# Kernel optimization log

Measured on AMD Instinct MI355X. Metric: run time of the kernel, lower is better.

The kernel has to match this reference:

```python
import jax, jax.numpy as jnp
import numpy as np

N = 2097152  # batch of 3x3 matrices


def setup_inputs() -> dict:
    key = jax.random.key(0)
    k1, k2 = jax.random.split(key)
    rotation = jax.random.normal(k1, (N, 3, 3), dtype=jnp.float32)
    # learned parameter: eye(3) + 1e-3 * randn, per __init__
    mat = jnp.eye(3, dtype=jnp.float32) + 0.001 * jax.random.normal(k2, (3, 3), dtype=jnp.float32)
    return {"rotation": rotation, "mat": mat}


def reference(rotation, mat):
    # new_mat = mat @ rotation (mat broadcast over batch)  -> [N,3,3]
    new_mat = jnp.einsum('ab,nbc->nac', mat, rotation)
    # polar rotation factor via batched 3x3 SVD: R = U @ V^T
    U, S, Vh = jnp.linalg.svd(new_mat, full_matrices=False)
    out = jnp.einsum('nab,nbc->nac', U, Vh)  # torch: U @ V.transpose == U @ Vh
    logdet = jnp.zeros((rotation.shape[0],), dtype=rotation.dtype)
    return out, logdet
```

## Files before the change

### kernel.cpp

```cpp
#include <hip/hip_runtime.h>
#include <math.h>


typedef float v2f __attribute__((ext_vector_type(2)));

#define NEWTON_ITERS 6
#define NS_ITERS 2

__global__ __launch_bounds__(256) void polar3x3_pk_kernel(
    const float* __restrict__ rot,
    const float* __restrict__ mat,
    float* __restrict__ out,
    int n)
{
    __shared__ float lds[4608];
    const int t = threadIdx.x;
    const long long base = (long long)blockIdx.x * 512;
    const bool full = (base + 512 <= (long long)n);

    if (full) {
        const float4* s4 = (const float4*)(rot + base * 9);
        float4* l4 = (float4*)lds;
        #pragma unroll
        for (int k = 0; k < 5; ++k) {
            int idx = t + 256 * k;
            if (idx < 1152) l4[idx] = s4[idx];
        }
    } else {
        for (int j = t; j < 4608; j += 256) {
            long long g = base * 9 + j;
            lds[j] = (g < (long long)n * 9) ? rot[g] : 0.0f;
        }
    }
    __syncthreads();

    const float* L = lds + t * 18;
    v2f r00 = {L[0], L[9]},  r01 = {L[1], L[10]}, r02 = {L[2], L[11]};
    v2f r10 = {L[3], L[12]}, r11 = {L[4], L[13]}, r12 = {L[5], L[14]};
    v2f r20 = {L[6], L[15]}, r21 = {L[7], L[16]}, r22 = {L[8], L[17]};

    const float m00 = mat[0], m01 = mat[1], m02 = mat[2];
    const float m10 = mat[3], m11 = mat[4], m12 = mat[5];
    const float m20 = mat[6], m21 = mat[7], m22 = mat[8];

    v2f x00 = m00*r00 + m01*r10 + m02*r20;
    v2f x01 = m00*r01 + m01*r11 + m02*r21;
    v2f x02 = m00*r02 + m01*r12 + m02*r22;
    v2f x10 = m10*r00 + m11*r10 + m12*r20;
    v2f x11 = m10*r01 + m11*r11 + m12*r21;
    v2f x12 = m10*r02 + m11*r12 + m12*r22;
    v2f x20 = m20*r00 + m21*r10 + m22*r20;
    v2f x21 = m20*r01 + m21*r11 + m22*r21;
    v2f x22 = m20*r02 + m21*r12 + m22*r22;

    #pragma unroll
    for (int it = 0; it < NEWTON_ITERS; ++it) {
        v2f c00 = x11*x22 - x12*x21;
        v2f c01 = x12*x20 - x10*x22;
        v2f c02 = x10*x21 - x11*x20;
        v2f c10 = x02*x21 - x01*x22;
        v2f c11 = x00*x22 - x02*x20;
        v2f c12 = x01*x20 - x00*x21;
        v2f c20 = x01*x12 - x02*x11;
        v2f c21 = x02*x10 - x00*x12;
        v2f c22 = x00*x11 - x01*x10;

        v2f det = x00*c00 + x01*c01 + x02*c02;

        float d0 = det.x, d1 = det.y;
        float ad0 = fmaxf(fabsf(d0), 1e-30f);
        float ad1 = fmaxf(fabsf(d1), 1e-30f);
        float z0 = __builtin_amdgcn_exp2f(__builtin_amdgcn_logf(ad0) * (-1.0f/3.0f));
        float z1 = __builtin_amdgcn_exp2f(__builtin_amdgcn_logf(ad1) * (-1.0f/3.0f));
        v2f s = {0.5f * z0, 0.5f * z1};
        v2f u = {copysignf(0.5f * z0 * z0, d0), copysignf(0.5f * z1 * z1, d1)};

        x00 = s*x00 + u*c00;  x01 = s*x01 + u*c01;  x02 = s*x02 + u*c02;
        x10 = s*x10 + u*c10;  x11 = s*x11 + u*c11;  x12 = s*x12 + u*c12;
        x20 = s*x20 + u*c20;  x21 = s*x21 + u*c21;  x22 = s*x22 + u*c22;
    }

    #pragma unroll
    for (int it = 0; it < NS_ITERS; ++it) {
        v2f s00 = x00*x00 + x10*x10 + x20*x20;
        v2f s01 = x00*x01 + x10*x11 + x20*x21;
        v2f s02 = x00*x02 + x10*x12 + x20*x22;
        v2f s11 = x01*x01 + x11*x11 + x21*x21;
        v2f s12 = x01*x02 + x11*x12 + x21*x22;
        v2f s22 = x02*x02 + x12*x12 + x22*x22;
        v2f t00 = 1.5f - 0.5f*s00, t01 = -0.5f*s01, t02 = -0.5f*s02;
        v2f t11 = 1.5f - 0.5f*s11, t12 = -0.5f*s12;
        v2f t22 = 1.5f - 0.5f*s22;
        v2f y00 = x00*t00 + x01*t01 + x02*t02;
        v2f y01 = x00*t01 + x01*t11 + x02*t12;
        v2f y02 = x00*t02 + x01*t12 + x02*t22;
        v2f y10 = x10*t00 + x11*t01 + x12*t02;
        v2f y11 = x10*t01 + x11*t11 + x12*t12;
        v2f y12 = x10*t02 + x11*t12 + x12*t22;
        v2f y20 = x20*t00 + x21*t01 + x22*t02;
        v2f y21 = x20*t01 + x21*t11 + x22*t12;
        v2f y22 = x20*t02 + x21*t12 + x22*t22;
        x00=y00; x01=y01; x02=y02;
        x10=y10; x11=y11; x12=y12;
        x20=y20; x21=y21; x22=y22;
    }

    float* S = lds + t * 18;
    S[0]=x00.x; S[9]=x00.y;  S[1]=x01.x; S[10]=x01.y;  S[2]=x02.x; S[11]=x02.y;
    S[3]=x10.x; S[12]=x10.y; S[4]=x11.x; S[13]=x11.y;  S[5]=x12.x; S[14]=x12.y;
    S[6]=x20.x; S[15]=x20.y; S[7]=x21.x; S[16]=x21.y;  S[8]=x22.x; S[17]=x22.y;
    __syncthreads();

    if (full) {
        float4* d4 = (float4*)(out + base * 9);
        const float4* l4 = (const float4*)lds;
        #pragma unroll
        for (int k = 0; k < 5; ++k) {
            int idx = t + 256 * k;
            if (idx < 1152) d4[idx] = l4[idx];
        }
        if (t < 128) {
            float4* ld4 = (float4*)(out + (long long)n * 9 + base);
            ld4[t] = make_float4(0.f, 0.f, 0.f, 0.f);
        }
    } else {
        for (int j = t; j < 4608; j += 256) {
            long long g = base * 9 + j;
            if (g < (long long)n * 9) out[g] = lds[j];
        }
        for (int j = t; j < 512; j += 256) {
            long long i2 = base + j;
            if (i2 < (long long)n) out[(long long)n * 9 + i2] = 0.0f;
        }
    }
}

extern "C" void kernel_launch(void* const* d_in, const int* in_sizes, int n_in,
                              void* d_out, int out_size, void* d_ws, size_t ws_size,
                              hipStream_t stream) {
    const float* rot = (const float*)d_in[0];
    const float* mat = (const float*)d_in[1];
    float* out = (float*)d_out;

    int n = in_sizes[0] / 9;
    int block = 256;
    int grid = (n + 511) / 512;
    polar3x3_pk_kernel<<<grid, block, 0, stream>>>(rot, mat, out, n);
}
```

Measured before the change: 32.33 us.

## Stage input per wavefront via global_load_lds and drop block barriers

Each wavefront now stages its own 128 matrices into a private LDS slice using direct global-to-LDS loads. This replaces the block-wide cooperative copy and removes both __syncthreads, relying on wave-local s_waitcnt instead. Output is written back through the wave's LDS slice with nontemporal vector stores. The tail path uses direct per-thread global access. This cuts block-level synchronisation and register staging, at the cost of relying on the semantics of global_load_lds and on intra-wave LDS ordering without an explicit barrier.

After: 29.70 us. 1.09x faster.

```diff
diff --git a/kernel.cpp b/kernel.cpp
--- a/kernel.cpp
+++ b/kernel.cpp
@@ -3,56 +3,16 @@
 
 
 typedef float v2f __attribute__((ext_vector_type(2)));
+typedef float v4f __attribute__((ext_vector_type(4)));
 
 #define NEWTON_ITERS 6
 #define NS_ITERS 2
 
-__global__ __launch_bounds__(256) void polar3x3_pk_kernel(
-    const float* __restrict__ rot,
-    const float* __restrict__ mat,
-    float* __restrict__ out,
-    int n)
+__device__ __forceinline__ void polar_pair(
+    v2f& x00, v2f& x01, v2f& x02,
+    v2f& x10, v2f& x11, v2f& x12,
+    v2f& x20, v2f& x21, v2f& x22)
 {
-    __shared__ float lds[4608];
-    const int t = threadIdx.x;
-    const long long base = (long long)blockIdx.x * 512;
-    const bool full = (base + 512 <= (long long)n);
-
-    if (full) {
-        const float4* s4 = (const float4*)(rot + base * 9);
-        float4* l4 = (float4*)lds;
-        #pragma unroll
-        for (int k = 0; k < 5; ++k) {
-            int idx = t + 256 * k;
-            if (idx < 1152) l4[idx] = s4[idx];
-        }
-    } else {
-        for (int j = t; j < 4608; j += 256) {
-            long long g = base * 9 + j;
-            lds[j] = (g < (long long)n * 9) ? rot[g] : 0.0f;
-        }
-    }
-    __syncthreads();
-
-    const float* L = lds + t * 18;
-    v2f r00 = {L[0], L[9]},  r01 = {L[1], L[10]}, r02 = {L[2], L[11]};
-    v2f r10 = {L[3], L[12]}, r11 = {L[4], L[13]}, r12 = {L[5], L[14]};
-    v2f r20 = {L[6], L[15]}, r21 = {L[7], L[16]}, r22 = {L[8], L[17]};
-
-    const float m00 = mat[0], m01 = mat[1], m02 = mat[2];
-    const float m10 = mat[3], m11 = mat[4], m12 = mat[5];
-    const float m20 = mat[6], m21 = mat[7], m22 = mat[8];
-
-    v2f x00 = m00*r00 + m01*r10 + m02*r20;
-    v2f x01 = m00*r01 + m01*r11 + m02*r21;
-    v2f x02 = m00*r02 + m01*r12 + m02*r22;
-    v2f x10 = m10*r00 + m11*r10 + m12*r20;
-    v2f x11 = m10*r01 + m11*r11 + m12*r21;
-    v2f x12 = m10*r02 + m11*r12 + m12*r22;
-    v2f x20 = m20*r00 + m21*r10 + m22*r20;
-    v2f x21 = m20*r01 + m21*r11 + m22*r21;
-    v2f x22 = m20*r02 + m21*r12 + m22*r22;
-
     #pragma unroll
     for (int it = 0; it < NEWTON_ITERS; ++it) {
         v2f c00 = x11*x22 - x12*x21;
@@ -104,33 +64,108 @@
         x10=y10; x11=y11; x12=y12;
         x20=y20; x21=y21; x22=y22;
     }
+}
 
-    float* S = lds + t * 18;
-    S[0]=x00.x; S[9]=x00.y;  S[1]=x01.x; S[10]=x01.y;  S[2]=x02.x; S[11]=x02.y;
-    S[3]=x10.x; S[12]=x10.y; S[4]=x11.x; S[13]=x11.y;  S[5]=x12.x; S[14]=x12.y;
-    S[6]=x20.x; S[15]=x20.y; S[7]=x21.x; S[16]=x21.y;  S[8]=x22.x; S[17]=x22.y;
-    __syncthreads();
+__global__ __launch_bounds__(256) void polar3x3_wave_kernel(
+    const float* __restrict__ rot,
+    const float* __restrict__ mat,
+    float* __restrict__ out,
+    int n)
+{
+    __shared__ float lds[4608];
+    const int t    = threadIdx.x;
+    const int lane = t & 63;
+    const int w    = t >> 6;
+    const long long blockBase = (long long)blockIdx.x * 512;
+    const long long waveBase  = blockBase + (long long)w * 128;
+    float* wlds = lds + w * 1152;
+
+    const float m00 = mat[0], m01 = mat[1], m02 = mat[2];
+    const float m10 = mat[3], m11 = mat[4], m12 = mat[5];
+    const float m20 = mat[6], m21 = mat[7], m22 = mat[8];
+
+    const bool full = (blockBase + 512 <= (long long)n);
+
+    v2f r00, r01, r02, r10, r11, r12, r20, r21, r22;
 
     if (full) {
-        float4* d4 = (float4*)(out + base * 9);
-        const float4* l4 = (const float4*)lds;
+        const float* gsrc = rot + waveBase * 9;
         #pragma unroll
-        for (int k = 0; k < 5; ++k) {
-            int idx = t + 256 * k;
-            if (idx < 1152) d4[idx] = l4[idx];
+        for (int k = 0; k < 4; ++k) {
+            __builtin_amdgcn_global_load_lds(
+                (const __attribute__((address_space(1))) void*)(gsrc + k * 256 + lane * 4),
+                (__attribute__((address_space(3))) void*)(wlds + k * 256),
+                16, 0, 0);
         }
-        if (t < 128) {
-            float4* ld4 = (float4*)(out + (long long)n * 9 + base);
-            ld4[t] = make_float4(0.f, 0.f, 0.f, 0.f);
+        #pragma unroll
+        for (int k = 0; k < 2; ++k) {
+            __builtin_amdgcn_global_load_lds(
+                (const __attribute__((address_space(1))) void*)(gsrc + 1024 + k * 64 + lane),
+                (__attribute__((address_space(3))) void*)(wlds + 1024 + k * 64),
+                4, 0, 0);
         }
+        asm volatile("s_waitcnt vmcnt(0)" ::: "memory");
+
+        const float* L = wlds + lane * 18;
+        r00 = v2f{L[0], L[9]};  r01 = v2f{L[1], L[10]}; r02 = v2f{L[2], L[11]};
+        r10 = v2f{L[3], L[12]}; r11 = v2f{L[4], L[13]}; r12 = v2f{L[5], L[14]};
+        r20 = v2f{L[6], L[15]}; r21 = v2f{L[7], L[16]}; r22 = v2f{L[8], L[17]};
     } else {
-        for (int j = t; j < 4608; j += 256) {
-            long long g = base * 9 + j;
-            if (g < (long long)n * 9) out[g] = lds[j];
+        #pragma unroll
+        for (int q = 0; q < 2; ++q) {
+            long long mi = waveBase + 2 * lane + q;
+            if (mi < (long long)n) {
+                const float* r = rot + mi * 9;
+                r00[q]=r[0]; r01[q]=r[1]; r02[q]=r[2];
+                r10[q]=r[3]; r11[q]=r[4]; r12[q]=r[5];
+                r20[q]=r[6]; r21[q]=r[7]; r22[q]=r[8];
+            } else {
+                r00[q]=1.f; r01[q]=0.f; r02[q]=0.f;
+                r10[q]=0.f; r11[q]=1.f; r12[q]=0.f;
+                r20[q]=0.f; r21[q]=0.f; r22[q]=1.f;
+            }
         }
-        for (int j = t; j < 512; j += 256) {
-            long long i2 = base + j;
-            if (i2 < (long long)n) out[(long long)n * 9 + i2] = 0.0f;
+    }
+
+    v2f x00 = m00*r00 + m01*r10 + m02*r20;
+    v2f x01 = m00*r01 + m01*r11 + m02*r21;
+    v2f x02 = m00*r02 + m01*r12 + m02*r22;
+    v2f x10 = m10*r00 + m11*r10 + m12*r20;
+    v2f x11 = m10*r01 + m11*r11 + m12*r21;
+    v2f x12 = m10*r02 + m11*r12 + m12*r22;
+    v2f x20 = m20*r00 + m21*r10 + m22*r20;
+    v2f x21 = m20*r01 + m21*r11 + m22*r21;
+    v2f x22 = m20*r02 + m21*r12 + m22*r22;
+
+    polar_pair(x00,x01,x02,x10,x11,x12,x20,x21,x22);
+
+    if (full) {
+        float* S = wlds + lane * 18;
+        S[0]=x00.x; S[9]=x00.y;  S[1]=x01.x; S[10]=x01.y;  S[2]=x02.x; S[11]=x02.y;
+        S[3]=x10.x; S[12]=x10.y; S[4]=x11.x; S[13]=x11.y;  S[5]=x12.x; S[14]=x12.y;
+        S[6]=x20.x; S[15]=x20.y; S[7]=x21.x; S[16]=x21.y;  S[8]=x22.x; S[17]=x22.y;
+        v4f* gdst4 = (v4f*)(out + waveBase * 9);
+        const v4f* l4 = (const v4f*)wlds;
+        #pragma unroll
+        for (int k = 0; k < 4; ++k)
+            __builtin_nontemporal_store(l4[k * 64 + lane], gdst4 + k * 64 + lane);
+        v2f* gdst2 = (v2f*)(out + waveBase * 9 + 1024);
+        const v2f* l2 = (const v2f*)(wlds + 1024);
+        __builtin_nontemporal_store(l2[lane], gdst2 + lane);
+
+        v2f* ld2 = (v2f*)(out + (long long)n * 9 + waveBase);
+        __builtin_nontemporal_store(v2f{0.f, 0.f}, ld2 + lane);
+    } else {
+        #pragma unroll
+        for (int q = 0; q < 2; ++q) {
+            long long mi = waveBase + 2 * lane + q;
+            if (mi < (long long)n) {
+                float* o = out + mi * 9;
+                o[0]=x00[q]; o[1]=x01[q]; o[2]=x02[q];
+                o[3]=x10[q]; o[4]=x11[q]; o[5]=x12[q];
+                o[6]=x20[q]; o[7]=x21[q]; o[8]=x22[q];
+                out[(long long)n * 9 + mi] = 0.0f;
+            }
         }
     }
 }
@@ -145,5 +180,5 @@
     int n = in_sizes[0] / 9;
     int block = 256;
     int grid = (n + 511) / 512;
-    polar3x3_pk_kernel<<<grid, block, 0, stream>>>(rot, mat, out, n);
+    polar3x3_wave_kernel<<<grid, block, 0, stream>>>(rot, mat, out, n);
 }
```
